# Optimization experiments

Hardware: AMD Instinct MI355X
Metric: run time of the kernel (lower is better)

The kernel has to match this reference:

```python
import jax, jax.numpy as jnp
import numpy as np
from jax import lax

IMSIZE = 4096
LINEWIDTH = 31  # odd, matches torch init adjustment


def _gen_kernel(lw):
    # Nested concentric squares: layer i covers [i, lw-i) with value (i+1)/(center+1);
    # inner layers overwrite outer ones, so value = (center - chebyshev_r + 1)/(center+1).
    c = lw // 2
    idx = jnp.arange(lw)
    r = jnp.maximum(jnp.abs(idx[:, None] - c), jnp.abs(idx[None, :] - c))
    val = (c - r + 1).astype(jnp.float32) / jnp.float32(c + 1)
    return jnp.broadcast_to(val, (3, 3, lw, lw))


def _rasterize(x0, y0, x1, y1, imsize):
    # Faithful port of the torch Bresenham variant (including the inner while loop).
    # All coordinate math is non-differentiable in the original (done via .data),
    # so we stop gradients here.
    x0 = lax.stop_gradient(x0)
    y0 = lax.stop_gradient(y0)
    x1 = lax.stop_gradient(x1)
    y1 = lax.stop_gradient(y1)
    dx = jnp.abs(x1 - x0)
    dy = jnp.abs(y1 - y0)
    sx = jnp.where(x1 > x0, 1.0, -1.0)
    sy = jnp.where(y1 > y0, 1.0, -1.0)
    steep = dy > dx
    # swap (x0,y0), (dx,dy), (sx,sy) when steep
    a = jnp.where(steep, y0, x0)
    b = jnp.where(steep, x0, y0)
    dX = jnp.where(steep, dy, dx)
    dY = jnp.where(steep, dx, dy)
    sa = jnp.where(steep, sy, sx)
    sb = jnp.where(steep, sx, sy)
    d = 2.0 * dY - dX
    n = dX.astype(jnp.int32)
    mask0 = jnp.zeros((imsize, imsize), dtype=jnp.float32)

    def body(i, carry):
        a, b, d, mask = carry
        row = jnp.where(steep, b, a).astype(jnp.int32)
        col = jnp.where(steep, a, b).astype(jnp.int32)
        mask = mask.at[row, col].set(1.0)

        def inner(bd):
            bb, dd = bd
            return (bb + sb, dd - 2.0 * dX)

        b, d = lax.while_loop(lambda bd: bd[1] >= 0.0, inner, (b, d))
        a = a + sa
        d = d + 2.0 * dY
        return (a, b, d, mask)

    _, _, _, mask = lax.fori_loop(0, n, body, (a, b, d, mask0))
    mask = mask.at[x1.astype(jnp.int32), y1.astype(jnp.int32)].set(1.0)
    return mask


def setup_inputs() -> dict:
    return {
        "x0": jnp.array([100.0], dtype=jnp.float32),
        "y0": jnp.array([200.0], dtype=jnp.float32),
        "x1": jnp.array([3900.0], dtype=jnp.float32),
        "y1": jnp.array([3500.0], dtype=jnp.float32),
    }


def reference(x0, y0, x1, y1):
    imsize, lw = IMSIZE, LINEWIDTH
    mask = _rasterize(x0[0], y0[0], x1[0], y1[0], imsize)  # [H, W]
    img = jnp.broadcast_to(mask, (1, 3, imsize, imsize))   # NCHW
    kernel = _gen_kernel(lw)                               # OIHW [3,3,lw,lw]
    pad = lw // 2
    out = lax.conv_general_dilated(
        img, kernel, window_strides=(1, 1),
        padding=[(pad, pad), (pad, pad)],
        dimension_numbers=("NCHW", "OIHW", "NCHW"))
    tmin = jnp.min(out)
    tmax = jnp.max(out)
    out = (out - tmin) / (tmax - tmin)
    return 1.0 - out[0]  # [3, imsize, imsize]
```

## Files before the change

### kernel.cpp

```cpp
#include <hip/hip_runtime.h>
#include <cstdint>
#include <cstddef>

#define IMSIZE 4096
#define HALF 15
#define SENT (-100000)

__global__ __launch_bounds__(1024) void k_line(
    const float* __restrict__ x0p, const float* __restrict__ y0p,
    const float* __restrict__ x1p, const float* __restrict__ y1p,
    int* __restrict__ hdr, int* __restrict__ map)
{
    int t = threadIdx.x;
    for (int i = t; i < IMSIZE; i += 1024) map[i] = SENT;
    __syncthreads();

    float x0 = x0p[0], y0 = y0p[0], x1 = x1p[0], y1 = y1p[0];
    float dx = fabsf(x1 - x0), dy = fabsf(y1 - y0);
    float sx = (x1 > x0) ? 1.f : -1.f;
    float sy = (y1 > y0) ? 1.f : -1.f;
    bool steep = dy > dx;
    float a0 = steep ? y0 : x0;
    float b0 = steep ? x0 : y0;
    float dX = steep ? dy : dx;
    float dY = steep ? dx : dy;
    float sa = steep ? sy : sx;
    float sb = steep ? sx : sy;
    int n = (int)dX;

    if (t == 0) { hdr[0] = steep ? 1 : 0; hdr[1] = 0; }

    double twodY = 2.0 * (double)dY;
    double twodX = 2.0 * (double)dX;
    double ddX   = (double)dX;
    for (int i = t; i < n; i += 1024) {
        int ki = (int)floor((twodY * (double)i + ddX) / twodX);
        float ai = a0 + sa * (float)i;
        float bi = b0 + sb * (float)ki;
        int M  = (int)ai;
        int mn = (int)bi;
        if ((unsigned)M < IMSIZE) map[M] = mn;
    }
    if (t == 0) {
        int M  = steep ? (int)y1 : (int)x1;
        int mn = steep ? (int)x1 : (int)y1;
        if ((unsigned)M < IMSIZE) map[M] = mn;
    }
}

__global__ __launch_bounds__(64) void k_band(
    int* __restrict__ hdr, const int* __restrict__ map,
    int* __restrict__ lo, int* __restrict__ hi)
{
    int M = blockIdx.x;
    int t = threadIdx.x;

    int v = SENT;
    if (t < 2 * HALF + 1) {
        int m = M - HALF + t;
        if ((unsigned)m < IMSIZE) v = map[m];
    }
    int vmin = (v <= SENT / 2) ? 0x7fffffff : v;
    int vmax = (v <= SENT / 2) ? (-0x7fffffff - 1) : v;
    #pragma unroll
    for (int o = 32; o >= 1; o >>= 1) {
        vmin = min(vmin, __shfl_xor(vmin, o));
        vmax = max(vmax, __shfl_xor(vmax, o));
    }
    int L, H;
    if (vmin == 0x7fffffff) { L = 1; H = 0; }
    else { L = max(vmin - HALF, 0); H = min(vmax + HALF, IMSIZE - 1); }
    if (t == 0) { lo[M] = L; hi[M] = H; }

    int smax = 0;
    for (int j = L + t; j <= H; j += 64) {
        int s = 0;
        #pragma unroll
        for (int dm = -HALF; dm <= HALF; ++dm) {
            int m = M + dm;
            if ((unsigned)m < IMSIZE) {
                int c = map[m];
                int ad = abs(c - j);
                if (ad <= HALF) s += 16 - max(ad, (dm < 0 ? -dm : dm));
            }
        }
        smax = max(smax, s);
    }
    #pragma unroll
    for (int o = 32; o >= 1; o >>= 1) smax = max(smax, __shfl_xor(smax, o));
    if (t == 0 && smax > 0) atomicMax(hdr + 1, smax);
}

__device__ __forceinline__ int conv_s(int i, int j, int steep,
                                      const int* __restrict__ map)
{
    int M  = steep ? j : i;
    int mn = steep ? i : j;
    int s = 0;
    #pragma unroll
    for (int dm = -HALF; dm <= HALF; ++dm) {
        int m = M + dm;
        if ((unsigned)m < IMSIZE) {
            int c = map[m];
            int ad = abs(c - mn);
            if (ad <= HALF) s += 16 - max(ad, (dm < 0 ? -dm : dm));
        }
    }
    return s;
}

__global__ __launch_bounds__(256) void k_write(
    const int* __restrict__ hdr, const int* __restrict__ map,
    const int* __restrict__ lo, const int* __restrict__ hi,
    float* __restrict__ out)
{
    int idx = blockIdx.x * 256 + threadIdx.x;
    int i  = idx >> 10;
    int j0 = (idx & 1023) << 2;
    int steep = hdr[0];
    float inv = 1.0f / (float)hdr[1];

    float4 v = make_float4(1.f, 1.f, 1.f, 1.f);
    float* vp = &v.x;
    if (!steep) {
        int L = lo[i], H = hi[i];
        if (j0 <= H && j0 + 3 >= L) {
            #pragma unroll
            for (int k = 0; k < 4; ++k) {
                int j = j0 + k;
                if (j >= L && j <= H) {
                    int s = conv_s(i, j, 0, map);
                    vp[k] = 1.0f - (float)s * inv;
                }
            }
        }
    } else {
        #pragma unroll
        for (int k = 0; k < 4; ++k) {
            int j = j0 + k;
            if (i >= lo[j] && i <= hi[j]) {
                int s = conv_s(i, j, 1, map);
                vp[k] = 1.0f - (float)s * inv;
            }
        }
    }

    const size_t CH4 = (size_t)IMSIZE * IMSIZE / 4;
    float4* o = (float4*)out;
    o[idx]            = v;
    o[idx + CH4]      = v;
    o[idx + 2 * CH4]  = v;
}

extern "C" void kernel_launch(void* const* d_in, const int* in_sizes, int n_in,
                              void* d_out, int out_size, void* d_ws, size_t ws_size,
                              hipStream_t stream)
{
    const float* x0 = (const float*)d_in[0];
    const float* y0 = (const float*)d_in[1];
    const float* x1 = (const float*)d_in[2];
    const float* y1 = (const float*)d_in[3];

    int* ws  = (int*)d_ws;
    int* hdr = ws;
    int* map = ws + 16;
    int* lo  = ws + 16 + IMSIZE;
    int* hi  = ws + 16 + 2 * IMSIZE;
    float* out = (float*)d_out;

    hipLaunchKernelGGL(k_line,  dim3(1),                   dim3(1024), 0, stream,
                       x0, y0, x1, y1, hdr, map);
    hipLaunchKernelGGL(k_band,  dim3(IMSIZE),              dim3(64),   0, stream,
                       hdr, map, lo, hi);
    hipLaunchKernelGGL(k_write, dim3(IMSIZE * 1024 / 256), dim3(256),  0, stream,
                       hdr, map, lo, hi, out);
}
```

Measured before the change: 258.6 us.

## Split output write into constant fill plus band-only patch kernel

The single full-image write kernel, which checked band bounds and ran the convolution per pixel, is replaced by two kernels. A plain kernel fills all three channels with 1.0, then a per-row kernel walks only the nonzero band of each row and overwrites those pixels with the normalized convolution value. The goal is to make the bulk of the work a branch-free streaming store and to confine the compute to the band. In exchange it adds a kernel launch, writes the band pixels twice, and uses scattered scalar stores in the patch kernel, which become strided when the line is steep.

Result: faster. 250.7 us (-3.0%).

```diff
diff --git a/kernel.cpp b/kernel.cpp
--- a/kernel.cpp
+++ b/kernel.cpp
@@ -48,6 +48,24 @@
     }
 }
 
+__device__ __forceinline__ int conv_s(int i, int j, int steep,
+                                      const int* __restrict__ map)
+{
+    int M  = steep ? j : i;
+    int mn = steep ? i : j;
+    int s = 0;
+    #pragma unroll
+    for (int dm = -HALF; dm <= HALF; ++dm) {
+        int m = M + dm;
+        if ((unsigned)m < IMSIZE) {
+            int c = map[m];
+            int ad = abs(c - mn);
+            if (ad <= HALF) s += 16 - max(ad, (dm < 0 ? -dm : dm));
+        }
+    }
+    return s;
+}
+
 __global__ __launch_bounds__(64) void k_band(
     int* __restrict__ hdr, const int* __restrict__ map,
     int* __restrict__ lo, int* __restrict__ hi)
@@ -72,84 +90,46 @@
     else { L = max(vmin - HALF, 0); H = min(vmax + HALF, IMSIZE - 1); }
     if (t == 0) { lo[M] = L; hi[M] = H; }
 
+    int steep = hdr[0];
     int smax = 0;
     for (int j = L + t; j <= H; j += 64) {
-        int s = 0;
-        #pragma unroll
-        for (int dm = -HALF; dm <= HALF; ++dm) {
-            int m = M + dm;
-            if ((unsigned)m < IMSIZE) {
-                int c = map[m];
-                int ad = abs(c - j);
-                if (ad <= HALF) s += 16 - max(ad, (dm < 0 ? -dm : dm));
-            }
-        }
-        smax = max(smax, s);
+        int row = steep ? j : M;
+        int col = steep ? M : j;
+        smax = max(smax, conv_s(row, col, steep, map));
     }
     #pragma unroll
     for (int o = 32; o >= 1; o >>= 1) smax = max(smax, __shfl_xor(smax, o));
     if (t == 0 && smax > 0) atomicMax(hdr + 1, smax);
 }
 
-__device__ __forceinline__ int conv_s(int i, int j, int steep,
-                                      const int* __restrict__ map)
+__global__ __launch_bounds__(256) void k_fill(float4* __restrict__ out)
 {
-    int M  = steep ? j : i;
-    int mn = steep ? i : j;
-    int s = 0;
-    #pragma unroll
-    for (int dm = -HALF; dm <= HALF; ++dm) {
-        int m = M + dm;
-        if ((unsigned)m < IMSIZE) {
-            int c = map[m];
-            int ad = abs(c - mn);
-            if (ad <= HALF) s += 16 - max(ad, (dm < 0 ? -dm : dm));
-        }
-    }
-    return s;
+    size_t idx = (size_t)blockIdx.x * 256 + threadIdx.x;
+    out[idx] = make_float4(1.f, 1.f, 1.f, 1.f);
 }
 
-__global__ __launch_bounds__(256) void k_write(
+__global__ __launch_bounds__(64) void k_patch(
     const int* __restrict__ hdr, const int* __restrict__ map,
     const int* __restrict__ lo, const int* __restrict__ hi,
     float* __restrict__ out)
 {
-    int idx = blockIdx.x * 256 + threadIdx.x;
-    int i  = idx >> 10;
-    int j0 = (idx & 1023) << 2;
+    int M = blockIdx.x;
+    int t = threadIdx.x;
+    int L = lo[M], H = hi[M];
     int steep = hdr[0];
     float inv = 1.0f / (float)hdr[1];
+    const size_t CH = (size_t)IMSIZE * IMSIZE;
 
-    float4 v = make_float4(1.f, 1.f, 1.f, 1.f);
-    float* vp = &v.x;
-    if (!steep) {
-        int L = lo[i], H = hi[i];
-        if (j0 <= H && j0 + 3 >= L) {
-            #pragma unroll
-            for (int k = 0; k < 4; ++k) {
-                int j = j0 + k;
-                if (j >= L && j <= H) {
-                    int s = conv_s(i, j, 0, map);
-                    vp[k] = 1.0f - (float)s * inv;
-                }
-            }
-        }
-    } else {
-        #pragma unroll
-        for (int k = 0; k < 4; ++k) {
-            int j = j0 + k;
-            if (i >= lo[j] && i <= hi[j]) {
-                int s = conv_s(i, j, 1, map);
-                vp[k] = 1.0f - (float)s * inv;
-            }
-        }
+    for (int j = L + t; j <= H; j += 64) {
+        int row = steep ? j : M;
+        int col = steep ? M : j;
+        int s = conv_s(row, col, steep, map);
+        float val = 1.0f - (float)s * inv;
+        size_t p = (size_t)row * IMSIZE + col;
+        out[p]          = val;
+        out[p + CH]     = val;
+        out[p + 2 * CH] = val;
     }
-
-    const size_t CH4 = (size_t)IMSIZE * IMSIZE / 4;
-    float4* o = (float4*)out;
-    o[idx]            = v;
-    o[idx + CH4]      = v;
-    o[idx + 2 * CH4]  = v;
 }
 
 extern "C" void kernel_launch(void* const* d_in, const int* in_sizes, int n_in,
@@ -168,10 +148,14 @@
     int* hi  = ws + 16 + 2 * IMSIZE;
     float* out = (float*)d_out;
 
-    hipLaunchKernelGGL(k_line,  dim3(1),                   dim3(1024), 0, stream,
+    const int NF4 = 3 * IMSIZE * IMSIZE / 4;
+
+    hipLaunchKernelGGL(k_fill,  dim3(NF4 / 256), dim3(256),  0, stream,
+                       (float4*)out);
+    hipLaunchKernelGGL(k_line,  dim3(1),         dim3(1024), 0, stream,
                        x0, y0, x1, y1, hdr, map);
-    hipLaunchKernelGGL(k_band,  dim3(IMSIZE),              dim3(64),   0, stream,
+    hipLaunchKernelGGL(k_band,  dim3(IMSIZE),    dim3(64),   0, stream,
                        hdr, map, lo, hi);
-    hipLaunchKernelGGL(k_write, dim3(IMSIZE * 1024 / 256), dim3(256),  0, stream,
+    hipLaunchKernelGGL(k_patch, dim3(IMSIZE),    dim3(64),   0, stream,
                        hdr, map, lo, hi, out);
 }
```
